# Kernel optimization log

Hardware: AMD Instinct MI355X
Metric: run time of the kernel (lower is better)

## Reference

```python
import jax, jax.numpy as jnp
import numpy as np

N_NODES = 10000
N_EDGES = 160000
IN_C = 32
OUT_C = 32
FC = 32
DIM = 3
RADIUS = 1.0
LN_EPS = 1e-5


def _layernorm(x, g, b):
    mu = jnp.mean(x, axis=-1, keepdims=True)
    var = jnp.mean(jnp.square(x - mu), axis=-1, keepdims=True)
    return (x - mu) * jax.lax.rsqrt(var + LN_EPS) * g + b


def setup_inputs() -> dict:
    key = jax.random.key(0)
    ks = jax.random.split(key, 10)
    inp = {
        "features": jax.random.normal(ks[0], (N_NODES, IN_C), dtype=jnp.float32),
        "hood_coords": jax.random.normal(ks[1], (N_EDGES, DIM), dtype=jnp.float32),
        "source": jax.random.randint(ks[2], (N_EDGES,), 0, N_NODES, dtype=jnp.int32),
        "target": jax.random.randint(ks[3], (N_EDGES,), 0, N_NODES, dtype=jnp.int32),
        # neural field params: Linear(DIM,FC) -> LN -> ReLU -> Linear(FC,FC) -> LN -> ReLU -> Linear(FC, IN_C*OUT_C) -> Tanh
        "W0": jax.random.normal(ks[4], (DIM, FC), dtype=jnp.float32) * 0.3,
        "b0": jnp.zeros((FC,), dtype=jnp.float32),
        "g0": jnp.ones((FC,), dtype=jnp.float32),
        "beta0": jnp.zeros((FC,), dtype=jnp.float32),
        "W1": jax.random.normal(ks[5], (FC, FC), dtype=jnp.float32) * 0.15,
        "b1": jnp.zeros((FC,), dtype=jnp.float32),
        "g1": jnp.ones((FC,), dtype=jnp.float32),
        "beta1": jnp.zeros((FC,), dtype=jnp.float32),
        "W2": jax.random.normal(ks[6], (FC, IN_C * OUT_C), dtype=jnp.float32) * 0.15,
        "b2": jnp.zeros((IN_C * OUT_C,), dtype=jnp.float32),
    }
    return inp


def reference(features, hood_coords, source, target,
              W0, b0, g0, beta0, W1, b1, g1, beta1, W2, b2):
    m = features.shape[0]
    # neural field: per-edge weight matrix w [E, OUT_C, IN_C]
    x = hood_coords / RADIUS
    h = jax.nn.relu(_layernorm(x @ W0 + b0, g0, beta0))
    h = jax.nn.relu(_layernorm(h @ W1 + b1, g1, beta1))
    w = jnp.tanh(h @ W2 + b2).reshape(-1, OUT_C, IN_C)
    # gather + batched matvec: out[e,o] = sum_i f[e,i] * w[e,o,i]
    f = features[source]
    oc = jnp.einsum('ni,noi->no', f, w)
    # scatter_mean over target nodes
    sums = jax.ops.segment_sum(oc, target, num_segments=m)
    counts = jax.ops.segment_sum(jnp.ones((target.shape[0],), dtype=oc.dtype),
                                 target, num_segments=m)
    counts = jnp.maximum(counts, 1.0)
    return sums / counts[:, None]
```

## Files before the change

### kernel.cpp

```cpp
#include <hip/hip_runtime.h>

#define LN_EPS 1e-5f

typedef __attribute__((ext_vector_type(8)))  short short8;
typedef __attribute__((ext_vector_type(4)))  float floatx4;
typedef __attribute__((ext_vector_type(16))) float floatx16;

__device__ __forceinline__ unsigned short f2bf(float x) {
    unsigned u = __float_as_uint(x);
    u += 0x7FFFu + ((u >> 16) & 1u);
    return (unsigned short)(u >> 16);
}

__global__ __launch_bounds__(256) void k_edge_mlp(
    const float* __restrict__ coords,
    const int*   __restrict__ target,
    const float* __restrict__ W0, const float* __restrict__ b0,
    const float* __restrict__ g0, const float* __restrict__ be0,
    const float* __restrict__ W1, const float* __restrict__ b1,
    const float* __restrict__ g1, const float* __restrict__ be1,
    const float* __restrict__ W2, unsigned short* __restrict__ w2frag,
    unsigned short* __restrict__ hfrag, int* __restrict__ counts,
    int E, int nEB)
{
    const int tid = threadIdx.x;

    if (blockIdx.x >= nEB) {
        const int idx = (blockIdx.x - nEB) * 256 + tid;
        if (idx < 4096) {
            const int l  = idx & 63;
            const int ot = idx >> 6;
            const int t  = ot & 1;
            const int o  = ot >> 1;
            const int row = l & 31;
            const int kb  = t*16 + (l >> 5)*8;
            short8 v;
            #pragma unroll
            for (int b = 0; b < 8; ++b)
                v[b] = (short)f2bf(W2[(size_t)(kb + b)*1024 + o*32 + row]);
            ((short8*)w2frag)[idx] = v;
        }
        return;
    }

    __shared__ float sW0[3*32], sW1[32*32];
    __shared__ float sb0[32], sg0[32], sbe0[32], sb1[32], sg1[32], sbe1[32];
    for (int i = tid; i < 32*32; i += 256) sW1[i] = W1[i];
    if (tid < 96) sW0[tid] = W0[tid];
    if (tid < 32) {
        sb0[tid] = b0[tid];  sg0[tid] = g0[tid];  sbe0[tid] = be0[tid];
        sb1[tid] = b1[tid];  sg1[tid] = g1[tid];  sbe1[tid] = be1[tid];
    }
    __syncthreads();

    const int e = blockIdx.x * 256 + tid;
    if (e >= E) return;

    const float x0 = coords[e*3+0];
    const float x1 = coords[e*3+1];
    const float x2 = coords[e*3+2];

    float h[32];
    #pragma unroll
    for (int o = 0; o < 32; ++o)
        h[o] = x0*sW0[o] + x1*sW0[32+o] + x2*sW0[64+o] + sb0[o];

    {
        float mu = 0.f;
        #pragma unroll
        for (int o = 0; o < 32; ++o) mu += h[o];
        mu *= (1.f/32.f);
        float var = 0.f;
        #pragma unroll
        for (int o = 0; o < 32; ++o) { float d = h[o]-mu; var += d*d; }
        var *= (1.f/32.f);
        const float inv = rsqrtf(var + LN_EPS);
        #pragma unroll
        for (int o = 0; o < 32; ++o)
            h[o] = fmaxf((h[o]-mu)*inv*sg0[o] + sbe0[o], 0.f);
    }

    float h2[32];
    #pragma unroll
    for (int o = 0; o < 32; ++o) {
        float s = sb1[o];
        #pragma unroll
        for (int c = 0; c < 32; ++c) s += h[c]*sW1[c*32+o];
        h2[o] = s;
    }

    {
        float mu = 0.f;
        #pragma unroll
        for (int o = 0; o < 32; ++o) mu += h2[o];
        mu *= (1.f/32.f);
        float var = 0.f;
        #pragma unroll
        for (int o = 0; o < 32; ++o) { float d = h2[o]-mu; var += d*d; }
        var *= (1.f/32.f);
        const float inv = rsqrtf(var + LN_EPS);
        #pragma unroll
        for (int o = 0; o < 32; ++o)
            h2[o] = fmaxf((h2[o]-mu)*inv*sg1[o] + sbe1[o], 0.f);
    }

    const int et = e >> 5, er = e & 31;
    short8* base = (short8*)(hfrag) + (size_t)et * 128;
    #pragma unroll
    for (int t = 0; t < 2; ++t) {
        #pragma unroll
        for (int kg = 0; kg < 2; ++kg) {
            short8 v;
            #pragma unroll
            for (int b = 0; b < 8; ++b) v[b] = (short)f2bf(h2[t*16 + kg*8 + b]);
            base[t*64 + kg*32 + er] = v;
        }
    }

    atomicAdd(&counts[target[e]], 1);
}

__global__ __launch_bounds__(1024) void k_scan(
    const int* __restrict__ counts, int* __restrict__ offs,
    int* __restrict__ cursor, int N)
{
    __shared__ int wsum[16];
    const int t = threadIdx.x;
    const int lane = t & 63, w = t >> 6;
    const int CH = (N + 1023) >> 10;
    const int beg = t * CH;

    int s = 0;
    for (int k = 0; k < CH; ++k) {
        const int i = beg + k;
        if (i < N) s += counts[i];
    }
    int incl = s;
    #pragma unroll
    for (int d = 1; d < 64; d <<= 1) {
        const int x = __shfl_up(incl, d);
        if (lane >= d) incl += x;
    }
    if (lane == 63) wsum[w] = incl;
    __syncthreads();
    if (t == 0) {
        int run = 0;
        #pragma unroll
        for (int i = 0; i < 16; ++i) { const int v = wsum[i]; wsum[i] = run; run += v; }
    }
    __syncthreads();
    const int base = wsum[w] + incl - s;
    int run = base;
    for (int k = 0; k < CH; ++k) {
        const int i = beg + k;
        if (i < N) { offs[i] = run; cursor[i] = run; run += counts[i]; }
    }
    if (t == 1023) offs[N] = base + s;
}

__global__ __launch_bounds__(256) void k_bucket(
    const int* __restrict__ tgt, int* __restrict__ cursor,
    int* __restrict__ pos, int E)
{
    const int e = blockIdx.x * 256 + threadIdx.x;
    if (e < E) pos[e] = atomicAdd(&cursor[tgt[e]], 1);
}

__global__ __launch_bounds__(512, 2) void k_field_mfma(
    const unsigned short* __restrict__ hfrag,
    const unsigned short* __restrict__ w2frag,
    const float* __restrict__ features,
    const int*   __restrict__ src,
    const int*   __restrict__ pos,
    const float* __restrict__ b2,
    unsigned short* __restrict__ ocP,
    int netiles)
{
    __shared__ float s_b2s[1024];
    __shared__ unsigned int sOC[32*17];
    __shared__ int sP[32];
    const int tid = threadIdx.x;
    const float KE = 2.8853900817779268f;
    s_b2s[tid]       = KE * b2[tid];
    s_b2s[tid + 512] = KE * b2[tid + 512];

    const int lane = tid & 63;
    const int w    = tid >> 6;
    const int h5   = lane >> 5;
    const int ecol = lane & 31;
    const float* b2base = &s_b2s[w*128 + 4*h5];
    const int str = tid >> 4;
    const int sti = tid & 15;

    short8 afr[8];
    #pragma unroll
    for (int u = 0; u < 8; ++u)
        afr[u] = ((const short8*)w2frag)[(w*8 + u)*64 + lane];
    __syncthreads();

    const floatx16 z16 = {0.f,0.f,0.f,0.f,0.f,0.f,0.f,0.f,
                          0.f,0.f,0.f,0.f,0.f,0.f,0.f,0.f};

    for (int et = blockIdx.x; et < netiles; et += gridDim.x) {
        const int e0 = et << 5;
        const short8 bs0 = ((const short8*)hfrag)[et*128 + lane];
        const short8 bs1 = ((const short8*)hfrag)[et*128 + 64 + lane];

        const int sN = src[e0 + ecol];
        const int p  = pos[e0 + ecol];
        if (tid < 32) sP[ecol] = p;

        floatx4 fv[4];
        float fsl = 0.f;
        #pragma unroll
        for (int rq = 0; rq < 4; ++rq) {
            fv[rq] = *reinterpret_cast<const floatx4*>(
                         features + (size_t)sN*32 + rq*8 + 4*h5);
            #pragma unroll
            for (int rr = 0; rr < 4; ++rr) fsl += fv[rq][rr];
        }

        float q[4];
        #pragma unroll
        for (int u = 0; u < 4; ++u) {
            floatx16 d = __builtin_amdgcn_mfma_f32_32x32x16_bf16(afr[2*u],   bs0, z16, 0, 0, 0);
            d          = __builtin_amdgcn_mfma_f32_32x32x16_bf16(afr[2*u+1], bs1, d,   0, 0, 0);
            float sf = 0.f;
            #pragma unroll
            for (int qq = 0; qq < 4; ++qq) {
                const floatx4 bq = *reinterpret_cast<const floatx4*>(b2base + u*32 + 8*qq);
                #pragma unroll
                for (int i = 0; i < 4; ++i) {
                    const float t = fmaf(d[qq*4 + i], KE, bq[i]);
                    const float r = __builtin_amdgcn_rcpf(__builtin_amdgcn_exp2f(t) + 1.0f);
                    sf = fmaf(fv[qq][i], r, sf);
                }
            }
            const float v = fmaf(-2.0f, sf, fsl);
            q[u] = v + __shfl_xor(v, 32);
        }

        if (lane < 32) {
            const unsigned d0 = ((unsigned)f2bf(q[1]) << 16) | f2bf(q[0]);
            const unsigned d1 = ((unsigned)f2bf(q[3]) << 16) | f2bf(q[2]);
            sOC[ecol*17 + w*2]     = d0;
            sOC[ecol*17 + w*2 + 1] = d1;
        }
        __syncthreads();
        ((unsigned int*)ocP)[(size_t)sP[str]*16 + sti] = sOC[str*17 + sti];
        __syncthreads();
    }
}

__global__ __launch_bounds__(256) void k_gather(
    const unsigned short* __restrict__ ocP,
    const int* __restrict__ offs,
    float* __restrict__ out, int N)
{
    const int node = blockIdx.x * 4 + (threadIdx.x >> 6);
    const int lane = threadIdx.x & 63;
    if (node >= N) return;
    const int r = lane >> 3;
    const int c = lane & 7;
    const int beg = offs[node], end = offs[node + 1];

    float a0 = 0.f, a1 = 0.f, a2 = 0.f, a3 = 0.f;
    for (int k = beg + r; k < end; k += 8) {
        const uint2 v = *reinterpret_cast<const uint2*>(ocP + (size_t)k*32 + c*4);
        a0 += __uint_as_float(v.x << 16);
        a1 += __uint_as_float(v.x & 0xFFFF0000u);
        a2 += __uint_as_float(v.y << 16);
        a3 += __uint_as_float(v.y & 0xFFFF0000u);
    }
    #pragma unroll
    for (int m = 8; m < 64; m <<= 1) {
        a0 += __shfl_xor(a0, m);
        a1 += __shfl_xor(a1, m);
        a2 += __shfl_xor(a2, m);
        a3 += __shfl_xor(a3, m);
    }
    if (lane < 8) {
        const float rinv = __builtin_amdgcn_rcpf(fmaxf((float)(end - beg), 1.0f));
        floatx4 o4 = {a0*rinv, a1*rinv, a2*rinv, a3*rinv};
        *reinterpret_cast<floatx4*>(out + (size_t)node*32 + lane*4) = o4;
    }
}

extern "C" void kernel_launch(void* const* d_in, const int* in_sizes, int n_in,
                              void* d_out, int out_size, void* d_ws, size_t ws_size,
                              hipStream_t stream)
{
    const float* features = (const float*)d_in[0];
    const float* coords   = (const float*)d_in[1];
    const int*   src      = (const int*)  d_in[2];
    const int*   tgt      = (const int*)  d_in[3];
    const float* W0  = (const float*)d_in[4];
    const float* b0  = (const float*)d_in[5];
    const float* g0  = (const float*)d_in[6];
    const float* be0 = (const float*)d_in[7];
    const float* W1  = (const float*)d_in[8];
    const float* b1  = (const float*)d_in[9];
    const float* g1  = (const float*)d_in[10];
    const float* be1 = (const float*)d_in[11];
    const float* W2  = (const float*)d_in[12];
    const float* b2  = (const float*)d_in[13];

    const int E = in_sizes[2];
    const int N = in_sizes[0] / 32;

    char* p = (char*)d_ws;
    unsigned short* hfrag  = (unsigned short*)p;  p += (size_t)E*32*2;
    unsigned short* ocP    = (unsigned short*)p;  p += (size_t)E*32*2;
    unsigned short* w2frag = (unsigned short*)p;  p += 32*1024*2;
    int* posArr = (int*)p;  p += (size_t)E*4;
    int* counts = (int*)p;  p += (size_t)N*4;
    int* cursor = (int*)p;  p += (size_t)N*4;
    int* offs   = (int*)p;  p += (size_t)(N+1)*4;

    (void)hipMemsetAsync(counts, 0, (size_t)N*4, stream);

    const int nEB = (E + 255)/256;
    k_edge_mlp<<<nEB + 16, 256, 0, stream>>>(
        coords, tgt, W0, b0, g0, be0, W1, b1, g1, be1, W2, w2frag,
        hfrag, counts, E, nEB);

    k_scan<<<1, 1024, 0, stream>>>(counts, offs, cursor, N);

    k_bucket<<<(E + 255)/256, 256, 0, stream>>>(tgt, cursor, posArr, E);

    const int netiles = E / 32;
    k_field_mfma<<<1024, 512, 0, stream>>>(
        hfrag, w2frag, features, src, posArr, b2, ocP, netiles);

    k_gather<<<(N + 3)/4, 256, 0, stream>>>(ocP, offs, (float*)d_out, N);
}
```

Baseline: 115.3 us.

## Split field MFMA tiles across half-blocks, double-buffer staging, transpose W1 in LDS

The field kernel now uses 256-thread blocks. Each block handles half of the 32 output-channel rows for an edge tile, chosen by blockIdx parity, giving twice as many work units and higher occupancy via launch bounds (256,6) and a 1536-block grid. The shared staging buffers are double-buffered so the trailing barrier can be dropped. The tanh/dot accumulation is split into four independent chains for more ILP. In the edge MLP, W1 is stored transposed and padded in shared memory so it can be read with vector loads. The cost is that the hfrag, feature-gather and src/pos loads are now repeated in both halves of every tile.

```diff
diff --git a/kernel.cpp b/kernel.cpp
--- a/kernel.cpp
+++ b/kernel.cpp
@@ -43,9 +43,12 @@
         return;
     }
 
-    __shared__ float sW0[3*32], sW1[32*32];
+    __shared__ float sW0[3*32], sW1T[32*36];
     __shared__ float sb0[32], sg0[32], sbe0[32], sb1[32], sg1[32], sbe1[32];
-    for (int i = tid; i < 32*32; i += 256) sW1[i] = W1[i];
+    for (int i = tid; i < 32*32; i += 256) {
+        const int o = i & 31, c = i >> 5;
+        sW1T[o*36 + c] = W1[i];
+    }
     if (tid < 96) sW0[tid] = W0[tid];
     if (tid < 32) {
         sb0[tid] = b0[tid];  sg0[tid] = g0[tid];  sbe0[tid] = be0[tid];
@@ -85,7 +88,11 @@
     for (int o = 0; o < 32; ++o) {
         float s = sb1[o];
         #pragma unroll
-        for (int c = 0; c < 32; ++c) s += h[c]*sW1[c*32+o];
+        for (int c4 = 0; c4 < 8; ++c4) {
+            const floatx4 wv = *reinterpret_cast<const floatx4*>(&sW1T[o*36 + c4*4]);
+            s += h[c4*4+0]*wv[0] + h[c4*4+1]*wv[1]
+               + h[c4*4+2]*wv[2] + h[c4*4+3]*wv[3];
+        }
         h2[o] = s;
     }
 
@@ -166,7 +173,7 @@
     if (e < E) pos[e] = atomicAdd(&cursor[tgt[e]], 1);
 }
 
-__global__ __launch_bounds__(512, 2) void k_field_mfma(
+__global__ __launch_bounds__(256, 6) void k_field_mfma(
     const unsigned short* __restrict__ hfrag,
     const unsigned short* __restrict__ w2frag,
     const float* __restrict__ features,
@@ -177,38 +184,43 @@
     int netiles)
 {
     __shared__ float s_b2s[1024];
-    __shared__ unsigned int sOC[32*17];
-    __shared__ int sP[32];
+    __shared__ unsigned int sOC[2][32*9];
+    __shared__ int sP[2][32];
     const int tid = threadIdx.x;
     const float KE = 2.8853900817779268f;
-    s_b2s[tid]       = KE * b2[tid];
-    s_b2s[tid + 512] = KE * b2[tid + 512];
+    #pragma unroll
+    for (int r = 0; r < 4; ++r) s_b2s[tid + 256*r] = KE * b2[tid + 256*r];
 
     const int lane = tid & 63;
-    const int w    = tid >> 6;
+    const int wq   = tid >> 6;
+    const int jh   = blockIdx.x & 1;
+    const int W    = jh*4 + wq;
     const int h5   = lane >> 5;
     const int ecol = lane & 31;
-    const float* b2base = &s_b2s[w*128 + 4*h5];
-    const int str = tid >> 4;
-    const int sti = tid & 15;
+    const float* b2base = &s_b2s[W*128 + 4*h5];
+    const int str = tid >> 3;
+    const int sti = tid & 7;
 
     short8 afr[8];
     #pragma unroll
     for (int u = 0; u < 8; ++u)
-        afr[u] = ((const short8*)w2frag)[(w*8 + u)*64 + lane];
+        afr[u] = ((const short8*)w2frag)[(W*8 + u)*64 + lane];
     __syncthreads();
 
     const floatx16 z16 = {0.f,0.f,0.f,0.f,0.f,0.f,0.f,0.f,
                           0.f,0.f,0.f,0.f,0.f,0.f,0.f,0.f};
 
-    for (int et = blockIdx.x; et < netiles; et += gridDim.x) {
+    const int nunits = 2*netiles;
+    int buf = 0;
+    for (int unit = blockIdx.x; unit < nunits; unit += gridDim.x, buf ^= 1) {
+        const int et = unit >> 1;
         const int e0 = et << 5;
         const short8 bs0 = ((const short8*)hfrag)[et*128 + lane];
         const short8 bs1 = ((const short8*)hfrag)[et*128 + 64 + lane];
 
         const int sN = src[e0 + ecol];
         const int p  = pos[e0 + ecol];
-        if (tid < 32) sP[ecol] = p;
+        if (tid < 32) sP[buf][ecol] = p;
 
         floatx4 fv[4];
         float fsl = 0.f;
@@ -225,30 +237,34 @@
         for (int u = 0; u < 4; ++u) {
             floatx16 d = __builtin_amdgcn_mfma_f32_32x32x16_bf16(afr[2*u],   bs0, z16, 0, 0, 0);
             d          = __builtin_amdgcn_mfma_f32_32x32x16_bf16(afr[2*u+1], bs1, d,   0, 0, 0);
-            float sf = 0.f;
+            float sf0 = 0.f, sf1 = 0.f, sf2 = 0.f, sf3 = 0.f;
             #pragma unroll
             for (int qq = 0; qq < 4; ++qq) {
                 const floatx4 bq = *reinterpret_cast<const floatx4*>(b2base + u*32 + 8*qq);
-                #pragma unroll
-                for (int i = 0; i < 4; ++i) {
-                    const float t = fmaf(d[qq*4 + i], KE, bq[i]);
-                    const float r = __builtin_amdgcn_rcpf(__builtin_amdgcn_exp2f(t) + 1.0f);
-                    sf = fmaf(fv[qq][i], r, sf);
+                {
+                    const float t0 = fmaf(d[qq*4+0], KE, bq[0]);
+                    sf0 = fmaf(fv[qq][0], __builtin_amdgcn_rcpf(__builtin_amdgcn_exp2f(t0) + 1.0f), sf0);
+                    const float t1 = fmaf(d[qq*4+1], KE, bq[1]);
+                    sf1 = fmaf(fv[qq][1], __builtin_amdgcn_rcpf(__builtin_amdgcn_exp2f(t1) + 1.0f), sf1);
+                    const float t2 = fmaf(d[qq*4+2], KE, bq[2]);
+                    sf2 = fmaf(fv[qq][2], __builtin_amdgcn_rcpf(__builtin_amdgcn_exp2f(t2) + 1.0f), sf2);
+                    const float t3 = fmaf(d[qq*4+3], KE, bq[3]);
+                    sf3 = fmaf(fv[qq][3], __builtin_amdgcn_rcpf(__builtin_amdgcn_exp2f(t3) + 1.0f), sf3);
                 }
             }
-            const float v = fmaf(-2.0f, sf, fsl);
+            const float sf = (sf0 + sf1) + (sf2 + sf3);
+            const float v  = fmaf(-2.0f, sf, fsl);
             q[u] = v + __shfl_xor(v, 32);
         }
 
         if (lane < 32) {
             const unsigned d0 = ((unsigned)f2bf(q[1]) << 16) | f2bf(q[0]);
             const unsigned d1 = ((unsigned)f2bf(q[3]) << 16) | f2bf(q[2]);
-            sOC[ecol*17 + w*2]     = d0;
-            sOC[ecol*17 + w*2 + 1] = d1;
+            sOC[buf][ecol*9 + wq*2]     = d0;
+            sOC[buf][ecol*9 + wq*2 + 1] = d1;
         }
         __syncthreads();
-        ((unsigned int*)ocP)[(size_t)sP[str]*16 + sti] = sOC[str*17 + sti];
-        __syncthreads();
+        ((unsigned int*)ocP)[(size_t)sP[buf][str]*16 + jh*8 + sti] = sOC[buf][str*9 + sti];
     }
 }
 
@@ -329,7 +345,7 @@
     k_bucket<<<(E + 255)/256, 256, 0, stream>>>(tgt, cursor, posArr, E);
 
     const int netiles = E / 32;
-    k_field_mfma<<<1024, 512, 0, stream>>>(
+    k_field_mfma<<<1536, 256, 0, stream>>>(
         hfrag, w2frag, features, src, posArr, b2, ocP, netiles);
 
     k_gather<<<(N + 3)/4, 256, 0, stream>>>(ocP, offs, (float*)d_out, N);
```

Result: slower. 196.5 us (+70.3%).
